# Performance work log

Measured on AMD Instinct MI355X. Metric: run time of the kernel, lower is better.

The kernel has to match this reference:

```python
import jax, jax.numpy as jnp
import numpy as np
from jax import lax

B, C, V, T = 8, 256, 96, 96
C8, C2 = C // 8, C // 2


def _conv3(x, w):
    # 3x3, stride 1, pad 1, no bias (the repo's misnamed 'conv1x1')
    return lax.conv_general_dilated(x, w, (1, 1), [(1, 1), (1, 1)],
                                    dimension_numbers=("NCHW", "OIHW", "NCHW"))


def _conv1(x, w, b):
    # true 1x1 conv with bias (cAttn q/k/v)
    y = lax.conv_general_dilated(x, w, (1, 1), [(0, 0), (0, 0)],
                                 dimension_numbers=("NCHW", "OIHW", "NCHW"))
    return y + b[None, :, None, None]


def setup_inputs() -> dict:
    key = jax.random.key(0)
    ks = jax.random.split(key, 20)
    s = 0.02
    d = {
        "x": jax.random.normal(ks[0], (B, C, V, T), jnp.float32),
        # vAttn (3x3 convs, no bias)
        "v_wq": jax.random.normal(ks[1], (C8, C, 3, 3), jnp.float32) * s,
        "v_wk": jax.random.normal(ks[2], (C8, C, 3, 3), jnp.float32) * s,
        "v_wv": jax.random.normal(ks[3], (C2, C, 3, 3), jnp.float32) * s,
        "v_wo": jax.random.normal(ks[4], (C, C2, 3, 3), jnp.float32) * s,
        "v_sigma": jax.random.normal(ks[5], (1,), jnp.float32),
        # tAttn
        "t_wq": jax.random.normal(ks[6], (C8, C, 3, 3), jnp.float32) * s,
        "t_wk": jax.random.normal(ks[7], (C8, C, 3, 3), jnp.float32) * s,
        "t_wv": jax.random.normal(ks[8], (C2, C, 3, 3), jnp.float32) * s,
        "t_wo": jax.random.normal(ks[9], (C, C2, 3, 3), jnp.float32) * s,
        "t_sigma": jax.random.normal(ks[10], (1,), jnp.float32),
        # cAttn (1x1 convs with bias for q/k/v, 3x3 for output proj)
        "c_wq": jax.random.normal(ks[11], (C, C, 1, 1), jnp.float32) * s,
        "c_bq": jax.random.normal(ks[12], (C,), jnp.float32) * s,
        "c_wk": jax.random.normal(ks[13], (C, C, 1, 1), jnp.float32) * s,
        "c_bk": jax.random.normal(ks[14], (C,), jnp.float32) * s,
        "c_wv": jax.random.normal(ks[15], (C, C, 1, 1), jnp.float32) * s,
        "c_bv": jax.random.normal(ks[16], (C,), jnp.float32) * s,
        "c_wo": jax.random.normal(ks[17], (C, C, 3, 3), jnp.float32) * s,
        "c_sigma": jax.random.normal(ks[18], (1,), jnp.float32),
    }
    return d


def reference(x, v_wq, v_wk, v_wv, v_wo, v_sigma,
              t_wq, t_wk, t_wv, t_wo, t_sigma,
              c_wq, c_bq, c_wk, c_bk, c_wv, c_bv, c_wo, c_sigma):
    # vAttn: attention over the v axis, independently per (b, t)
    q = _conv3(x, v_wq)                                   # [B,C8,V,T]
    k = _conv3(x, v_wk)
    v = _conv3(x, v_wv)                                   # [B,C2,V,T]
    a = jax.nn.softmax(jnp.einsum('bcvt,bcwt->btvw', q, k), axis=-1)
    av = jnp.einsum('btvw,bcwt->bcvt', a, v)              # [B,C2,V,T]
    x1 = v_sigma * _conv3(av, v_wo)

    # tAttn: attention over the t axis, independently per (b, v)
    q = _conv3(x, t_wq)
    k = _conv3(x, t_wk)
    v = _conv3(x, t_wv)
    a = jax.nn.softmax(jnp.einsum('bcvt,bcvs->bvts', q, k), axis=-1)
    av = jnp.einsum('bvts,bcvs->bcvt', a, v)
    x2 = t_sigma * _conv3(av, t_wo)

    # cAttn: attention over the channel axis, independently per (b, v)
    q = _conv1(x, c_wq, c_bq)                             # [B,C,V,T]
    k = _conv1(x, c_wk, c_bk)
    v = _conv1(x, c_wv, c_bv)
    a = jax.nn.softmax(jnp.einsum('bcvt,bdvt->bvcd', q, k), axis=-1)
    av = jnp.einsum('bvcd,bdvt->bcvt', a, v)
    x3 = c_sigma * _conv3(av, c_wo)

    return x + x1 + x2 + x3
```

## Files before the change

### kernel.cpp

```cpp
#include <hip/hip_runtime.h>
#include <math.h>

#define BB  8
#define CH  256
#define NVT 9216
#define PLN (98*98*32)
#define PROW (98*32)

typedef short bh8 __attribute__((ext_vector_type(8)));
typedef short bh4 __attribute__((ext_vector_type(4)));
typedef float f4  __attribute__((ext_vector_type(4)));

__device__ __forceinline__ float bf2f(ushort u) {
    union { uint i; float f; } x; x.i = ((uint)u) << 16; return x.f;
}
__device__ __forceinline__ ushort f2bf(float f) {
    union { float f; uint i; } x; x.f = f;
    uint r = (x.i + 0x7FFFu + ((x.i >> 16) & 1u)) >> 16;
    return (ushort)r;
}
__device__ __forceinline__ int cperm(int ci) {
    return 8 * ((ci >> 2) & 3) + 4 * (ci >> 4) + (ci & 3);
}
__device__ __forceinline__ void gld16(const void* g, void* l) {
    __builtin_amdgcn_global_load_lds(
        (const __attribute__((address_space(1))) void*)g,
        (__attribute__((address_space(3))) void*)l, 16, 0, 0);
}

__global__ __launch_bounds__(256) void pad_zero_k(ushort* __restrict__ x32,
                                                  ushort* __restrict__ avall)
{
    int p = blockIdx.x;
    ushort* base = (p < 64) ? x32 + (size_t)p * PLN
                            : avall + (size_t)(p - 64) * PLN;
    const bh8 z = {0,0,0,0,0,0,0,0};
    for (int n = threadIdx.x; n < 1552; n += 256) {
        size_t off;
        if (n < 392)       off = (size_t)n * 8;
        else if (n < 784)  off = (size_t)97 * PROW + (size_t)(n - 392) * 8;
        else {
            int m = n - 784;
            int vq = m >> 3, side = (m >> 2) & 1, sub = m & 3;
            off = ((size_t)(vq + 1) * 98 + side * 97) * 32 + sub * 8;
        }
        *(bh8*)&base[off] = z;
    }
}

__global__ __launch_bounds__(256) void cvt_x32_k(const float* __restrict__ x,
                                                 ushort* __restrict__ x32)
{
    __shared__ ushort tile[96 * 32];
    int v = blockIdx.x, kc = blockIdx.y, b = blockIdx.z;
    int ci = threadIdx.x >> 3, tp = threadIdx.x & 7;
    const float* src = x + (((size_t)(b * 256 + kc * 32 + ci)) * 96 + v) * 96 + tp * 12;
    int pc = cperm(ci);
    int gci = pc >> 3, idx = pc & 7;
#pragma unroll
    for (int u = 0; u < 12; ++u) {
        int t = tp * 12 + u;
        int sw = ((t + 1) >> 1) & 3;
        tile[t * 32 + 8 * (gci ^ sw) + idx] = f2bf(src[u]);
    }
    __syncthreads();
    ushort* dst = x32 + (((size_t)(b * 8 + kc) * 98 + v + 1) * 98 + 1) * 32;
    for (int n = threadIdx.x; n < 384; n += 256)
        *(bh8*)&dst[n * 8] = *(const bh8*)&tile[n * 8];
}

__global__ __launch_bounds__(256) void wpack_k(const float* __restrict__ w,
    ushort* __restrict__ dst, int CIN, int TAPS, int Csrc, int coBase, int COT,
    int kcBase, const float* __restrict__ scale)
{
    int n = blockIdx.x * 256 + threadIdx.x;
    int total = (CIN >> 5) * TAPS * Csrc * 32;
    if (n >= total) return;
    int kl  = n & 31;
    int rem = n >> 5;
    int col = rem % Csrc; rem /= Csrc;
    int tap = rem % TAPS;
    int kc  = rem / TAPS;
    int ci  = kc * 32 + kl;
    int g   = (kl >> 2) & 3;
    int i   = ((kl >> 4) << 2) | (kl & 3);
    int cog = coBase + col;
    int cot = cog >> 4, lc = cog & 15;
    float v = w[((size_t)col * CIN + ci) * TAPS + tap];
    if (scale) v *= scale[0];
    dst[((((size_t)(kcBase + kc) * TAPS + tap) * COT + cot) * 64 + (g * 16 + lc)) * 8 + i]
        = f2bf(v);
}

template<int TAPS, int CT, int OMODE>
__global__ __launch_bounds__(512, 2) void conv_mfma(
    const ushort* __restrict__ xin, const ushort* __restrict__ wpk,
    ushort* __restrict__ obf, const ushort* __restrict__ xres32,
    float* __restrict__ oacc, const float* __restrict__ bias,
    const float* __restrict__ bias2, int KC)
{
    constexpr int ROWS   = (TAPS == 9) ? 3 : 1;
    constexpr int SLABS  = ROWS * PROW;
    constexpr int CHUNKS = (SLABS * 2 + 1023) / 1024;
    constexpr int BUFSZ  = CHUNKS * 512;
    constexpr int COT    = CT * 4;
    constexpr int COUT   = COT * 16;
    __shared__ ushort sx[2][BUFSZ];

    const int v0 = blockIdx.x, b = blockIdx.y;
    const int tid = threadIdx.x;
    const int w = tid >> 6, l = tid & 63;
    const int g = l >> 4, lc = l & 15;
    const int wc = w & 3, wt = w >> 2;

    f4 acc[CT][3];
#pragma unroll
    for (int ct = 0; ct < CT; ++ct)
#pragma unroll
        for (int nt = 0; nt < 3; ++nt) acc[ct][nt] = (f4){0.f, 0.f, 0.f, 0.f};

    auto stage = [&](int kc, int buf) {
        const ushort* src = xin +
            (((size_t)b * KC + kc) * 98 + v0 + ((TAPS == 9) ? 0 : 1)) * (size_t)PROW;
#pragma unroll
        for (int c = 0; c < (CHUNKS + 7) / 8; ++c) {
            int ch = w + c * 8;
            if (ch < CHUNKS)
                gld16(src + ch * 512 + l * 8, &sx[buf][ch * 512 + l * 8]);
        }
    };

    stage(0, 0);
    __syncthreads();
    for (int kc = 0; kc < KC; ++kc) {
        const int cur = kc & 1;
        if (kc + 1 < KC) stage(kc + 1, cur ^ 1);
        const bh8* wp = (const bh8*)wpk;
#pragma unroll
        for (int tap = 0; tap < TAPS; ++tap) {
            const int kh = (TAPS == 9) ? tap / 3 : 0;
            const int kw = (TAPS == 9) ? tap % 3 : 1;
            bh8 af[CT];
#pragma unroll
            for (int ct = 0; ct < CT; ++ct)
                af[ct] = wp[(((size_t)kc * TAPS + tap) * COT + (wc * CT + ct)) * 64 + l];
#pragma unroll
            for (int nt = 0; nt < 3; ++nt) {
                int tp = wt * 48 + nt * 16 + lc + kw;
                bh8 bf = *(const bh8*)&sx[cur][(kh * 98 + tp) * 32
                                              + 8 * (g ^ ((tp >> 1) & 3))];
#pragma unroll
                for (int ct = 0; ct < CT; ++ct)
                    acc[ct][nt] = __builtin_amdgcn_mfma_f32_16x16x32_bf16(
                        af[ct], bf, acc[ct][nt], 0, 0, 0);
            }
        }
        __syncthreads();
    }

#pragma unroll
    for (int ct = 0; ct < CT; ++ct) {
#pragma unroll
        for (int nt = 0; nt < 3; ++nt) {
            int tt = wt * 48 + nt * 16 + lc;
            if (OMODE == 2) {
                bh4 o;
#pragma unroll
                for (int j = 0; j < 4; ++j) {
                    int cog = (wc * CT + ct) * 16 + g * 4 + j;
                    float val = acc[ct][nt][j];
                    if (bias) val += bias[cog];
                    o[j] = (short)f2bf(val);
                }
                *(bh4*)&obf[(((size_t)b * 96 + v0) * 96 + tt) * COUT
                            + (wc * CT + ct) * 16 + g * 4] = o;
            } else if (OMODE == 0) {
#pragma unroll
                for (int j = 0; j < 4; ++j) {
                    int cog = (wc * CT + ct) * 16 + g * 4 + j;
                    float val = acc[ct][nt][j];
                    if (bias) val += (cog < 256) ? bias[cog]
                                                : (bias2 ? bias2[cog - 256] : 0.f);
                    obf[(((size_t)b * COUT + cog) * 96 + v0) * 96 + tt] = f2bf(val);
                }
            } else {
                int cb  = (wc * CT + ct) * 16 + g * 4;
                int ci5 = cb & 31;
                int gci = (ci5 >> 2) & 3;
                int idx = 4 * (ci5 >> 4);
                int swr = ((1 + tt) >> 1) & 3;
                const ushort* xr = xres32 +
                    ((((size_t)b * 8 + (cb >> 5)) * 98 + 1 + v0) * 98 + 1 + tt) * 32;
                bh4 rv = *(const bh4*)&xr[8 * (gci ^ swr) + idx];
#pragma unroll
                for (int j = 0; j < 4; ++j) {
                    size_t o = (((size_t)b * COUT + cb + j) * 96 + v0) * 96 + tt;
                    oacc[o] = bf2f((ushort)rv[j]) + acc[ct][nt][j];
                }
            }
        }
    }
}

__global__ __launch_bounds__(256) void transpose_vt_k(const ushort* __restrict__ in,
                                                      ushort* __restrict__ out,
                                                      int cs_in, int cn)
{
    __shared__ ushort tile[96][100];
    int b = blockIdx.x / cn, c = blockIdx.x % cn;
    size_t sbase = ((size_t)b * cs_in + c) * NVT;
    size_t dbase = (size_t)blockIdx.x * NVT;
    for (int n = threadIdx.x; n < NVT; n += 256) tile[n / 96][n % 96] = in[sbase + n];
    __syncthreads();
    for (int n = threadIdx.x; n < NVT; n += 256) out[dbase + n] = tile[n % 96][n / 96];
}

template<bool OVER_V>
__global__ __launch_bounds__(384) void attn_vt_mfma_k(const ushort* __restrict__ qkv,
                                                      ushort* __restrict__ avall,
                                                      int sec, int cstride, int cbase)
{
    __shared__ ushort sQT[96 * 40];
    __shared__ ushort sKT[96 * 40];
    __shared__ ushort sV[128 * 104];

    int b = blockIdx.x / 96, p = blockIdx.x % 96;
    int tid = threadIdx.x;
    int wv = tid >> 6, l = tid & 63;
    int g = l >> 4, lc = l & 15;

    const size_t base = ((size_t)b * cstride + cbase) * (size_t)NVT + (size_t)p * 96;

    for (int s = tid; s < 768; s += 384) {
        int hf = s / 384;
        int c  = (s % 384) / 12;
        int m  = s % 12;
        bh8 val = *(const bh8*)&qkv[base + (size_t)(hf * 32 + c) * NVT + 8 * m];
        ushort* dst = hf ? sKT : sQT;
#pragma unroll
        for (int u = 0; u < 8; ++u)
            dst[(8 * m + u) * 40 + c] = (ushort)val[u];
    }
    for (int s = tid; s < 1536; s += 384) {
        int c = s / 12, m = s % 12;
        *(bh8*)&sV[c * 104 + 8 * m] =
            *(const bh8*)&qkv[base + (size_t)(64 + c) * NVT + 8 * m];
    }
    __syncthreads();

    bh4 qlo = *(const bh4*)&sQT[(wv * 16 + lc) * 40 + 4 * g];
    bh4 qhi = *(const bh4*)&sQT[(wv * 16 + lc) * 40 + 4 * g + 16];
    bh8 bq = __builtin_shufflevector(qlo, qhi, 0, 1, 2, 3, 4, 5, 6, 7);

    f4 st[6];
#pragma unroll
    for (int mt = 0; mt < 6; ++mt) {
        bh4 alo = *(const bh4*)&sKT[(mt * 16 + lc) * 40 + 4 * g];
        bh4 ahi = *(const bh4*)&sKT[(mt * 16 + lc) * 40 + 4 * g + 16];
        bh8 ak = __builtin_shufflevector(alo, ahi, 0, 1, 2, 3, 4, 5, 6, 7);
        st[mt] = __builtin_amdgcn_mfma_f32_16x16x32_bf16(ak, bq,
                                                         (f4){0.f, 0.f, 0.f, 0.f},
                                                         0, 0, 0);
    }

    float mx = -1e30f;
#pragma unroll
    for (int mt = 0; mt < 6; ++mt)
#pragma unroll
        for (int j = 0; j < 4; ++j) mx = fmaxf(mx, st[mt][j]);
    mx = fmaxf(mx, __shfl_xor(mx, 16));
    mx = fmaxf(mx, __shfl_xor(mx, 32));
    float sum = 0.f;
#pragma unroll
    for (int mt = 0; mt < 6; ++mt)
#pragma unroll
        for (int j = 0; j < 4; ++j) {
            float e = __expf(st[mt][j] - mx);
            st[mt][j] = e;
            sum += e;
        }
    sum += __shfl_xor(sum, 16);
    sum += __shfl_xor(sum, 32);
    float inv = 1.f / sum;

    bh8 pf[3];
#pragma unroll
    for (int ks = 0; ks < 3; ++ks) {
        bh8 t;
#pragma unroll
        for (int i = 0; i < 8; ++i)
            t[i] = (short)f2bf(st[2 * ks + (i >> 2)][i & 3] * inv);
        pf[ks] = t;
    }

    f4 acc[8];
#pragma unroll
    for (int mt = 0; mt < 8; ++mt) acc[mt] = (f4){0.f, 0.f, 0.f, 0.f};
#pragma unroll
    for (int ks = 0; ks < 3; ++ks)
#pragma unroll
        for (int mt = 0; mt < 8; ++mt) {
            bh4 alo = *(const bh4*)&sV[(mt * 16 + lc) * 104 + ks * 32 + 4 * g];
            bh4 ahi = *(const bh4*)&sV[(mt * 16 + lc) * 104 + ks * 32 + 4 * g + 16];
            bh8 avf = __builtin_shufflevector(alo, ahi, 0, 1, 2, 3, 4, 5, 6, 7);
            acc[mt] = __builtin_amdgcn_mfma_f32_16x16x32_bf16(avf, pf[ks],
                                                              acc[mt], 0, 0, 0);
        }

    int i = wv * 16 + lc;
#pragma unroll
    for (int mt = 0; mt < 8; ++mt) {
        int vv_ = OVER_V ? i : p;
        int tt_ = OVER_V ? p : i;
        int sw  = ((1 + tt_) >> 1) & 3;
        bh4 o;
#pragma unroll
        for (int j = 0; j < 4; ++j) o[j] = (short)f2bf(acc[mt][j]);
        size_t off = ((((size_t)b * 16 + sec + (mt >> 1)) * 98 + 1 + vv_) * 98
                      + 1 + tt_) * 32 + 8 * (g ^ sw) + 4 * (mt & 1);
        *(bh4*)&avall[off] = o;
    }
}

__global__ __launch_bounds__(256) void attn_c_k(const ushort* __restrict__ qkc,
    const ushort* __restrict__ vc, ushort* __restrict__ avall)
{
    __shared__ ushort sQ[64 * 104];
    __shared__ ushort sK[256 * 104];
    __shared__ ushort sV[96 * 264];
    __shared__ ushort sP[64 * 264];

    int v = blockIdx.x, cc = blockIdx.y, b = blockIdx.z;
    int c0 = cc * 64;
    int tid = threadIdx.x;
    int w = tid >> 6, l = tid & 63;
    int g = l >> 4, lc = l & 15;

    for (int s = tid; s < 64 * 12; s += 256) {
        int r = s / 12, sg = s % 12;
        *(bh8*)&sQ[r * 104 + sg * 8] =
            *(const bh8*)&qkc[(((size_t)b * 512 + c0 + r) * 96 + v) * 96 + sg * 8];
    }
    for (int s = tid; s < 256 * 12; s += 256) {
        int r = s / 12, sg = s % 12;
        *(bh8*)&sK[r * 104 + sg * 8] =
            *(const bh8*)&qkc[(((size_t)b * 512 + 256 + r) * 96 + v) * 96 + sg * 8];
    }
    for (int s = tid; s < 96 * 32; s += 256) {
        int r = s / 32, sg = s % 32;
        *(bh8*)&sV[r * 264 + sg * 8] =
            *(const bh8*)&vc[(((size_t)b * 96 + v) * 96 + r) * 256 + sg * 8];
    }
    __syncthreads();

    f4 s16[16];
#pragma unroll
    for (int nt = 0; nt < 16; ++nt) s16[nt] = (f4){0.f, 0.f, 0.f, 0.f};
#pragma unroll
    for (int ks = 0; ks < 3; ++ks) {
        bh4 alo = *(const bh4*)&sQ[(w * 16 + lc) * 104 + ks * 32 + 4 * g];
        bh4 ahi = *(const bh4*)&sQ[(w * 16 + lc) * 104 + ks * 32 + 4 * g + 16];
        bh8 aq = __builtin_shufflevector(alo, ahi, 0, 1, 2, 3, 4, 5, 6, 7);
#pragma unroll
        for (int nt = 0; nt < 16; ++nt) {
            bh4 blo = *(const bh4*)&sK[(nt * 16 + lc) * 104 + ks * 32 + 4 * g];
            bh4 bhi = *(const bh4*)&sK[(nt * 16 + lc) * 104 + ks * 32 + 4 * g + 16];
            bh8 bk = __builtin_shufflevector(blo, bhi, 0, 1, 2, 3, 4, 5, 6, 7);
            s16[nt] = __builtin_amdgcn_mfma_f32_16x16x32_bf16(aq, bk, s16[nt], 0, 0, 0);
        }
    }
#pragma unroll
    for (int j = 0; j < 4; ++j) {
        float m = -1e30f;
#pragma unroll
        for (int nt = 0; nt < 16; ++nt) m = fmaxf(m, s16[nt][j]);
        m = fmaxf(m, __shfl_xor(m, 1));
        m = fmaxf(m, __shfl_xor(m, 2));
        m = fmaxf(m, __shfl_xor(m, 4));
        m = fmaxf(m, __shfl_xor(m, 8));
        float sum = 0.f;
#pragma unroll
        for (int nt = 0; nt < 16; ++nt) {
            float e = __expf(s16[nt][j] - m); s16[nt][j] = e; sum += e;
        }
        sum += __shfl_xor(sum, 1);
        sum += __shfl_xor(sum, 2);
        sum += __shfl_xor(sum, 4);
        sum += __shfl_xor(sum, 8);
        float inv = 1.f / sum;
#pragma unroll
        for (int nt = 0; nt < 16; ++nt)
            sP[(w * 16 + g * 4 + j) * 264 + nt * 16 + lc] = f2bf(s16[nt][j] * inv);
    }
    __syncthreads();

    f4 o6[6];
#pragma unroll
    for (int nt = 0; nt < 6; ++nt) o6[nt] = (f4){0.f, 0.f, 0.f, 0.f};
#pragma unroll
    for (int ks = 0; ks < 8; ++ks) {
        bh4 alo = *(const bh4*)&sP[(w * 16 + lc) * 264 + ks * 32 + 4 * g];
        bh4 ahi = *(const bh4*)&sP[(w * 16 + lc) * 264 + ks * 32 + 4 * g + 16];
        bh8 ap = __builtin_shufflevector(alo, ahi, 0, 1, 2, 3, 4, 5, 6, 7);
#pragma unroll
        for (int nt = 0; nt < 6; ++nt) {
            bh4 blo = *(const bh4*)&sV[(nt * 16 + lc) * 264 + ks * 32 + 4 * g];
            bh4 bhi = *(const bh4*)&sV[(nt * 16 + lc) * 264 + ks * 32 + 4 * g + 16];
            bh8 bv = __builtin_shufflevector(blo, bhi, 0, 1, 2, 3, 4, 5, 6, 7);
            o6[nt] = __builtin_amdgcn_mfma_f32_16x16x32_bf16(ap, bv, o6[nt], 0, 0, 0);
        }
    }
#pragma unroll
    for (int nt = 0; nt < 6; ++nt) {
        int t = nt * 16 + lc;
        int sw = ((1 + t) >> 1) & 3;
        bh4 o;
#pragma unroll
        for (int j = 0; j < 4; ++j) o[j] = (short)f2bf(o6[nt][j]);
        size_t off = ((((size_t)b * 16 + 8 + cc * 2 + (w >> 1)) * 98 + 1 + v) * 98
                      + 1 + t) * 32 + 8 * (g ^ sw) + 4 * (w & 1);
        *(bh4*)&avall[off] = o;
    }
}

extern "C" void kernel_launch(void* const* d_in, const int* in_sizes, int n_in,
                              void* d_out, int out_size, void* d_ws, size_t ws_size,
                              hipStream_t stream)
{
    const float* x     = (const float*)d_in[0];
    const float* v_wq  = (const float*)d_in[1];
    const float* v_wk  = (const float*)d_in[2];
    const float* v_wv  = (const float*)d_in[3];
    const float* v_wo  = (const float*)d_in[4];
    const float* v_sig = (const float*)d_in[5];
    const float* t_wq  = (const float*)d_in[6];
    const float* t_wk  = (const float*)d_in[7];
    const float* t_wv  = (const float*)d_in[8];
    const float* t_wo  = (const float*)d_in[9];
    const float* t_sig = (const float*)d_in[10];
    const float* c_wq  = (const float*)d_in[11];
    const float* c_bq  = (const float*)d_in[12];
    const float* c_wk  = (const float*)d_in[13];
    const float* c_bk  = (const float*)d_in[14];
    const float* c_wv  = (const float*)d_in[15];
    const float* c_bv  = (const float*)d_in[16];
    const float* c_wo  = (const float*)d_in[17];
    const float* c_sig = (const float*)d_in[18];

    float*  out = (float*)d_out;
    ushort* ws  = (ushort*)d_ws;

    const size_t X32  = 0;
    const size_t AVL  = X32 + 19685376;
    const size_t POOL = AVL + 39354368;
    const size_t QKV   = POOL;
    const size_t QKVVT = POOL + 28311552;
    const size_t QKC   = POOL;
    const size_t VCT   = POOL + 37748736;
    const size_t PK    = POOL + 56623104;
    const size_t PK_PVT = PK;
    const size_t PK_CQK = PK_PVT + 884736;
    const size_t PK_CV  = PK_CQK + 131072;
    const size_t PK_FIN = PK_CV + 65536;

    pad_zero_k<<<192, 256, 0, stream>>>(ws + X32, ws + AVL);
    cvt_x32_k<<<dim3(96, 8, BB), 256, 0, stream>>>(x, ws + X32);

    auto pack = [&](const float* w, size_t dst, int cin, int taps, int csrc,
                    int cobase, int cot, int kcb, const float* sc) {
        int total = (cin >> 5) * taps * csrc * 32;
        wpack_k<<<(total + 255) / 256, 256, 0, stream>>>(w, ws + dst, cin, taps,
                                                          csrc, cobase, cot, kcb, sc);
    };
    pack(v_wq, PK_PVT, 256, 9, 32, 0, 24, 0, nullptr);
    pack(v_wk, PK_PVT, 256, 9, 32, 32, 24, 0, nullptr);
    pack(v_wv, PK_PVT, 256, 9, 128, 64, 24, 0, nullptr);
    pack(t_wq, PK_PVT, 256, 9, 32, 192, 24, 0, nullptr);
    pack(t_wk, PK_PVT, 256, 9, 32, 224, 24, 0, nullptr);
    pack(t_wv, PK_PVT, 256, 9, 128, 256, 24, 0, nullptr);
    pack(c_wq, PK_CQK, 256, 1, 256, 0, 32, 0, nullptr);
    pack(c_wk, PK_CQK, 256, 1, 256, 256, 32, 0, nullptr);
    pack(c_wv, PK_CV, 256, 1, 256, 0, 16, 0, nullptr);
    pack(v_wo, PK_FIN, 128, 9, 256, 0, 16, 0, v_sig);
    pack(t_wo, PK_FIN, 128, 9, 256, 0, 16, 4, t_sig);
    pack(c_wo, PK_FIN, 256, 9, 256, 0, 16, 8, c_sig);

    dim3 cgrid(96, BB);

    conv_mfma<9, 6, 0><<<cgrid, 512, 0, stream>>>(
        ws + X32, ws + PK_PVT, ws + QKV, nullptr, nullptr, nullptr, nullptr, 8);

    transpose_vt_k<<<BB * 192, 256, 0, stream>>>(ws + QKV, ws + QKVVT, 384, 192);
    attn_vt_mfma_k<true><<<BB * 96, 384, 0, stream>>>(ws + QKVVT, ws + AVL, 0, 192, 0);

    attn_vt_mfma_k<false><<<BB * 96, 384, 0, stream>>>(ws + QKV, ws + AVL, 4, 384, 192);

    conv_mfma<1, 8, 0><<<cgrid, 512, 0, stream>>>(
        ws + X32, ws + PK_CQK, ws + QKC, nullptr, nullptr, c_bq, c_bk, 8);
    conv_mfma<1, 4, 2><<<cgrid, 512, 0, stream>>>(
        ws + X32, ws + PK_CV, ws + VCT, nullptr, nullptr, c_bv, nullptr, 8);
    attn_c_k<<<dim3(96, 4, BB), 256, 0, stream>>>(ws + QKC, ws + VCT, ws + AVL);

    conv_mfma<9, 4, 5><<<cgrid, 512, 0, stream>>>(
        ws + AVL, ws + PK_FIN, nullptr, ws + X32, out, nullptr, nullptr, 16);
}
```

Measured before the change: 672.2 us.

## Merge cAttn q/k/v 1x1 convs into one kernel and tile final conv over two rows

The separate cAttn q/k and v 1x1 conv launches become one launch. It uses 8 column waves over 768 outputs, concatenated bias buffers, and a split epilogue that writes q/k channel-major and v token-major. The final 3x3 output conv now processes two v-rows per block, staging four input rows and reusing them across both rows, which halves the grid. This cuts redundant input staging and launch count, but raises per-thread accumulator count (more registers) and shrinks grid parallelism for the final conv.

```diff
diff --git a/kernel.cpp b/kernel.cpp
--- a/kernel.cpp
+++ b/kernel.cpp
@@ -92,32 +92,45 @@
         = f2bf(v);
 }
 
-template<int TAPS, int CT, int OMODE>
+__global__ __launch_bounds__(256) void bias3_k(const float* __restrict__ bq,
+    const float* __restrict__ bk, const float* __restrict__ bv,
+    float* __restrict__ o)
+{
+    int i = blockIdx.x * 256 + threadIdx.x;
+    if (i >= 768) return;
+    o[i] = (i < 256) ? bq[i] : (i < 512 ? bk[i - 256] : bv[i - 512]);
+}
+
+template<int TAPS, int CT, int OMODE, int NR, int NWC>
 __global__ __launch_bounds__(512, 2) void conv_mfma(
     const ushort* __restrict__ xin, const ushort* __restrict__ wpk,
-    ushort* __restrict__ obf, const ushort* __restrict__ xres32,
-    float* __restrict__ oacc, const float* __restrict__ bias,
-    const float* __restrict__ bias2, int KC)
-{
-    constexpr int ROWS   = (TAPS == 9) ? 3 : 1;
-    constexpr int SLABS  = ROWS * PROW;
-    constexpr int CHUNKS = (SLABS * 2 + 1023) / 1024;
-    constexpr int BUFSZ  = CHUNKS * 512;
-    constexpr int COT    = CT * 4;
-    constexpr int COUT   = COT * 16;
+    ushort* __restrict__ obf, ushort* __restrict__ aux,
+    float* __restrict__ oacc, const float* __restrict__ bias, int KC)
+{
+    constexpr int ROWS_ST = (TAPS == 9) ? (NR + 2) : NR;
+    constexpr int SLABS   = ROWS_ST * PROW;
+    constexpr int CHUNKS  = (SLABS * 2 + 1023) / 1024;
+    constexpr int BUFSZ   = CHUNKS * 512;
+    constexpr int COT     = NWC * CT;
+    constexpr int COUT    = COT * 16;
+    constexpr int NT      = (NWC == 8 || NR == 2) ? 6 : 3;
     __shared__ ushort sx[2][BUFSZ];
 
-    const int v0 = blockIdx.x, b = blockIdx.y;
+    const int v0 = blockIdx.x * NR, b = blockIdx.y;
     const int tid = threadIdx.x;
     const int w = tid >> 6, l = tid & 63;
     const int g = l >> 4, lc = l & 15;
-    const int wc = w & 3, wt = w >> 2;
-
-    f4 acc[CT][3];
+    const int wc = w % NWC, sub = w / NWC;
+    const int tbase = (NR == 1 && NWC == 4) ? sub * 48 : 0;
+    const int wr = (NR == 2) ? sub : 0;
+
+    f4 acc[CT][NT];
 #pragma unroll
     for (int ct = 0; ct < CT; ++ct)
 #pragma unroll
-        for (int nt = 0; nt < 3; ++nt) acc[ct][nt] = (f4){0.f, 0.f, 0.f, 0.f};
+        for (int nt = 0; nt < NT; ++nt) acc[ct][nt] = (f4){0.f, 0.f, 0.f, 0.f};
+
+    const bh8* wp0 = (const bh8*)wpk + (size_t)(wc * CT) * 64 + l;
 
     auto stage = [&](int kc, int buf) {
         const ushort* src = xin +
@@ -135,7 +148,6 @@
     for (int kc = 0; kc < KC; ++kc) {
         const int cur = kc & 1;
         if (kc + 1 < KC) stage(kc + 1, cur ^ 1);
-        const bh8* wp = (const bh8*)wpk;
 #pragma unroll
         for (int tap = 0; tap < TAPS; ++tap) {
             const int kh = (TAPS == 9) ? tap / 3 : 0;
@@ -143,11 +155,11 @@
             bh8 af[CT];
 #pragma unroll
             for (int ct = 0; ct < CT; ++ct)
-                af[ct] = wp[(((size_t)kc * TAPS + tap) * COT + (wc * CT + ct)) * 64 + l];
-#pragma unroll
-            for (int nt = 0; nt < 3; ++nt) {
-                int tp = wt * 48 + nt * 16 + lc + kw;
-                bh8 bf = *(const bh8*)&sx[cur][(kh * 98 + tp) * 32
+                af[ct] = wp0[(((size_t)kc * TAPS + tap) * COT + ct) * 64];
+#pragma unroll
+            for (int nt = 0; nt < NT; ++nt) {
+                int tp = tbase + nt * 16 + lc + kw;
+                bh8 bf = *(const bh8*)&sx[cur][(wr + kh) * PROW + tp * 32
                                               + 8 * (g ^ ((tp >> 1) & 3))];
 #pragma unroll
                 for (int ct = 0; ct < CT; ++ct)
@@ -158,30 +170,36 @@
         __syncthreads();
     }
 
+    const int rv = v0 + wr;
 #pragma unroll
     for (int ct = 0; ct < CT; ++ct) {
 #pragma unroll
-        for (int nt = 0; nt < 3; ++nt) {
-            int tt = wt * 48 + nt * 16 + lc;
-            if (OMODE == 2) {
-                bh4 o;
+        for (int nt = 0; nt < NT; ++nt) {
+            int tt = tbase + nt * 16 + lc;
+            if (OMODE == 0) {
 #pragma unroll
                 for (int j = 0; j < 4; ++j) {
                     int cog = (wc * CT + ct) * 16 + g * 4 + j;
                     float val = acc[ct][nt][j];
                     if (bias) val += bias[cog];
-                    o[j] = (short)f2bf(val);
+                    obf[(((size_t)b * COUT + cog) * 96 + rv) * 96 + tt] = f2bf(val);
                 }
-                *(bh4*)&obf[(((size_t)b * 96 + v0) * 96 + tt) * COUT
-                            + (wc * CT + ct) * 16 + g * 4] = o;
-            } else if (OMODE == 0) {
-#pragma unroll
-                for (int j = 0; j < 4; ++j) {
-                    int cog = (wc * CT + ct) * 16 + g * 4 + j;
-                    float val = acc[ct][nt][j];
-                    if (bias) val += (cog < 256) ? bias[cog]
-                                                : (bias2 ? bias2[cog - 256] : 0.f);
-                    obf[(((size_t)b * COUT + cog) * 96 + v0) * 96 + tt] = f2bf(val);
+            } else if (OMODE == 6) {
+                int cogb = (wc * CT + ct) * 16;
+                if (cogb < 512) {
+#pragma unroll
+                    for (int j = 0; j < 4; ++j) {
+                        int cog = cogb + g * 4 + j;
+                        float val = acc[ct][nt][j] + bias[cog];
+                        obf[(((size_t)b * 512 + cog) * 96 + rv) * 96 + tt] = f2bf(val);
+                    }
+                } else {
+                    bh4 o;
+#pragma unroll
+                    for (int j = 0; j < 4; ++j)
+                        o[j] = (short)f2bf(acc[ct][nt][j] + bias[cogb + g * 4 + j]);
+                    *(bh4*)&aux[(((size_t)b * 96 + rv) * 96 + tt) * 256
+                                + (cogb - 512) + g * 4] = o;
                 }
             } else {
                 int cb  = (wc * CT + ct) * 16 + g * 4;
@@ -189,13 +207,13 @@
                 int gci = (ci5 >> 2) & 3;
                 int idx = 4 * (ci5 >> 4);
                 int swr = ((1 + tt) >> 1) & 3;
-                const ushort* xr = xres32 +
-                    ((((size_t)b * 8 + (cb >> 5)) * 98 + 1 + v0) * 98 + 1 + tt) * 32;
-                bh4 rv = *(const bh4*)&xr[8 * (gci ^ swr) + idx];
+                const ushort* xr = aux +
+                    ((((size_t)b * 8 + (cb >> 5)) * 98 + 1 + rv) * 98 + 1 + tt) * 32;
+                bh4 rvv = *(const bh4*)&xr[8 * (gci ^ swr) + idx];
 #pragma unroll
                 for (int j = 0; j < 4; ++j) {
-                    size_t o = (((size_t)b * COUT + cb + j) * 96 + v0) * 96 + tt;
-                    oacc[o] = bf2f((ushort)rv[j]) + acc[ct][nt][j];
+                    size_t o = (((size_t)b * 256 + cb + j) * 96 + rv) * 96 + tt;
+                    oacc[o] = bf2f((ushort)rvv[j]) + acc[ct][nt][j];
                 }
             }
         }
@@ -459,12 +477,13 @@
     const size_t VCT   = POOL + 37748736;
     const size_t PK    = POOL + 56623104;
     const size_t PK_PVT = PK;
-    const size_t PK_CQK = PK_PVT + 884736;
-    const size_t PK_CV  = PK_CQK + 131072;
-    const size_t PK_FIN = PK_CV + 65536;
+    const size_t PK_C3  = PK_PVT + 884736;
+    const size_t PK_FIN = PK_C3 + 196608;
+    const size_t B3     = PK_FIN + 1179648;
 
     pad_zero_k<<<192, 256, 0, stream>>>(ws + X32, ws + AVL);
     cvt_x32_k<<<dim3(96, 8, BB), 256, 0, stream>>>(x, ws + X32);
+    bias3_k<<<3, 256, 0, stream>>>(c_bq, c_bk, c_bv, (float*)(ws + B3));
 
     auto pack = [&](const float* w, size_t dst, int cin, int taps, int csrc,
                     int cobase, int cot, int kcb, const float* sc) {
@@ -478,29 +497,26 @@
     pack(t_wq, PK_PVT, 256, 9, 32, 192, 24, 0, nullptr);
     pack(t_wk, PK_PVT, 256, 9, 32, 224, 24, 0, nullptr);
     pack(t_wv, PK_PVT, 256, 9, 128, 256, 24, 0, nullptr);
-    pack(c_wq, PK_CQK, 256, 1, 256, 0, 32, 0, nullptr);
-    pack(c_wk, PK_CQK, 256, 1, 256, 256, 32, 0, nullptr);
-    pack(c_wv, PK_CV, 256, 1, 256, 0, 16, 0, nullptr);
+    pack(c_wq, PK_C3, 256, 1, 256, 0, 48, 0, nullptr);
+    pack(c_wk, PK_C3, 256, 1, 256, 256, 48, 0, nullptr);
+    pack(c_wv, PK_C3, 256, 1, 256, 512, 48, 0, nullptr);
     pack(v_wo, PK_FIN, 128, 9, 256, 0, 16, 0, v_sig);
     pack(t_wo, PK_FIN, 128, 9, 256, 0, 16, 4, t_sig);
     pack(c_wo, PK_FIN, 256, 9, 256, 0, 16, 8, c_sig);
 
-    dim3 cgrid(96, BB);
-
-    conv_mfma<9, 6, 0><<<cgrid, 512, 0, stream>>>(
-        ws + X32, ws + PK_PVT, ws + QKV, nullptr, nullptr, nullptr, nullptr, 8);
+    conv_mfma<9, 6, 0, 1, 4><<<dim3(96, BB), 512, 0, stream>>>(
+        ws + X32, ws + PK_PVT, ws + QKV, nullptr, nullptr, nullptr, 8);
 
     transpose_vt_k<<<BB * 192, 256, 0, stream>>>(ws + QKV, ws + QKVVT, 384, 192);
     attn_vt_mfma_k<true><<<BB * 96, 384, 0, stream>>>(ws + QKVVT, ws + AVL, 0, 192, 0);
 
     attn_vt_mfma_k<false><<<BB * 96, 384, 0, stream>>>(ws + QKV, ws + AVL, 4, 384, 192);
 
-    conv_mfma<1, 8, 0><<<cgrid, 512, 0, stream>>>(
-        ws + X32, ws + PK_CQK, ws + QKC, nullptr, nullptr, c_bq, c_bk, 8);
-    conv_mfma<1, 4, 2><<<cgrid, 512, 0, stream>>>(
-        ws + X32, ws + PK_CV, ws + VCT, nullptr, nullptr, c_bv, nullptr, 8);
+    conv_mfma<1, 6, 6, 1, 8><<<dim3(96, BB), 512, 0, stream>>>(
+        ws + X32, ws + PK_C3, ws + QKC, ws + VCT, nullptr,
+        (const float*)(ws + B3), 8);
     attn_c_k<<<dim3(96, 4, BB), 256, 0, stream>>>(ws + QKC, ws + VCT, ws + AVL);
 
-    conv_mfma<9, 4, 5><<<cgrid, 512, 0, stream>>>(
-        ws + AVL, ws + PK_FIN, nullptr, ws + X32, out, nullptr, nullptr, 16);
-}
+    conv_mfma<9, 4, 5, 2, 4><<<dim3(48, BB), 512, 0, stream>>>(
+        ws + AVL, ws + PK_FIN, nullptr, ws + X32, out, nullptr, 16);
+}
```

Measured after the change: 626.5 us. 1.07x faster.
